# Optimization experiments

Measured on AMD Instinct MI355X. Metric: run time of the kernel, lower is better.

The kernel has to match this reference:

```python
import jax, jax.numpy as jnp
import numpy as np

H, D_IN, D_ATT, D_OUT, S, T = 16, 1024, 64, 64, 2048, 2048


def setup_inputs() -> dict:
    key = jax.random.key(0)
    ks = jax.random.split(key, 12)
    s = lambda fan_in: 1.0 / np.sqrt(fan_in)
    inp = {
        "current_tokens": jax.random.normal(ks[0], (S, D_IN), jnp.float32),
        "context_tokens": jax.random.normal(ks[1], (T, D_IN), jnp.float32),
        # per-head projection weights (stacked over heads)
        "Wq": jax.random.uniform(ks[2], (H, D_IN, D_ATT), jnp.float32, -s(D_IN), s(D_IN)),
        "bq": jax.random.uniform(ks[3], (H, D_ATT), jnp.float32, -s(D_IN), s(D_IN)),
        "Wk": jax.random.uniform(ks[4], (H, D_IN, D_ATT), jnp.float32, -s(D_IN), s(D_IN)),
        "bk": jax.random.uniform(ks[5], (H, D_ATT), jnp.float32, -s(D_IN), s(D_IN)),
        "Wv": jax.random.uniform(ks[6], (H, D_IN, D_OUT), jnp.float32, -s(D_IN), s(D_IN)),
        "bv": jax.random.uniform(ks[7], (H, D_OUT), jnp.float32, -s(D_IN), s(D_IN)),
        # out_proj: Linear(H*D_OUT -> D_OUT)
        "Wo": jax.random.uniform(ks[8], (H * D_OUT, D_OUT), jnp.float32, -s(H * D_OUT), s(H * D_OUT)),
        "bo": jax.random.uniform(ks[9], (D_OUT,), jnp.float32, -s(H * D_OUT), s(H * D_OUT)),
    }
    return inp


def reference(current_tokens, context_tokens, Wq, bq, Wk, bk, Wv, bv, Wo, bo):
    # Batched over heads: q,k: [H,S/T,D_ATT], v: [H,T,D_OUT]
    q = jnp.einsum("si,hid->hsd", current_tokens, Wq) + bq[:, None, :]
    k = jnp.einsum("ti,hid->htd", context_tokens, Wk) + bk[:, None, :]
    v = jnp.einsum("ti,hio->hto", context_tokens, Wv) + bv[:, None, :]
    scores = jnp.einsum("hsd,htd->hst", q, k) / jnp.sqrt(jnp.asarray(D_ATT, q.dtype))
    attn = jax.nn.softmax(scores, axis=-1)          # [H,S,T]
    y = jnp.einsum("hst,hto->hso", attn, v)          # [H,S,D_OUT]
    # torch.cat(ys, dim=0) -> [H*S, D_OUT]; .view(-1, H*D_OUT) -> [S, H*D_OUT]
    # (row-major reshape of head-major stacking, exactly as the torch code does)
    y = y.reshape(-1, D_OUT).reshape(-1, H * D_OUT)
    return y @ Wo + bo                               # [S, D_OUT]
```

## Files before the change

### kernel.cpp

```cpp
#include <hip/hip_runtime.h>

#define DEV static __device__ __forceinline__

typedef unsigned short u16;
typedef unsigned int u32;
typedef float f32x4 __attribute__((ext_vector_type(4)));
typedef __bf16 bf16x8 __attribute__((ext_vector_type(8)));
typedef unsigned short u16x8 __attribute__((ext_vector_type(8)));
typedef unsigned int u32x2 __attribute__((ext_vector_type(2)));
typedef unsigned int u32x4 __attribute__((ext_vector_type(4)));

constexpr int H = 16, DIN = 1024, DH = 64, S = 2048, T = 2048;
constexpr float SM_C = 0.18033688011112042f;

DEV u16 f2bf(float f) { return __builtin_bit_cast(u16, (__bf16)f); }
DEV float bf2f(u16 u) { u32 i = (u32)u << 16; return __builtin_bit_cast(float, i); }
DEV bf16x8 ld_bf8(const u16* p) { return __builtin_bit_cast(bf16x8, *(const u16x8*)p); }
DEV u32 cvtpk(float lo, float hi) {
  u32 r; asm("v_cvt_pk_bf16_f32 %0, %1, %2" : "=v"(r) : "v"(lo), "v"(hi)); return r;
}

#define GLOAD16(gp, lp) __builtin_amdgcn_global_load_lds( \
    (const __attribute__((address_space(1))) void*)(gp),  \
    (__attribute__((address_space(3))) void*)(lp), 16, 0, 0)

__global__ __launch_bounds__(256) void prep_kernel(
    const float* __restrict__ cur, const float* __restrict__ ctx,
    const float* __restrict__ Wq, const float* __restrict__ Wk,
    const float* __restrict__ Wv, const float* __restrict__ Wo,
    u16* __restrict__ cur_bf, u16* __restrict__ ctx_bf,
    u16* __restrict__ WqT, u16* __restrict__ WkvT, u16* __restrict__ WoT) {
  __shared__ alignas(16) float tile[64 * 68];
  int bid = blockIdx.x, tid = threadIdx.x;
  if (bid < 2048) {
    int i = bid * 256 + tid;
    const float* in; u16* out; int j;
    if (i < 262144) { in = cur; out = cur_bf; j = i; }
    else            { in = ctx; out = ctx_bf; j = i - 262144; }
    const float4* p = (const float4*)(in + (size_t)j * 8);
    float4 x = p[0], y = p[1];
    u16x8 o;
    o[0] = f2bf(x.x); o[1] = f2bf(x.y); o[2] = f2bf(x.z); o[3] = f2bf(x.w);
    o[4] = f2bf(y.x); o[5] = f2bf(y.y); o[6] = f2bf(y.z); o[7] = f2bf(y.w);
    *(u16x8*)(out + (size_t)j * 8) = o;
    return;
  }
  int t = bid - 2048, k0 = (t & 15) * 64, y = t >> 4;
  const float* W; u16* Wt; float scale = 1.0f;
  if (y < 16)      { W = Wq + (size_t)y * DIN * DH;        Wt = WqT + (size_t)y * DH * DIN; scale = SM_C; }
  else if (y < 32) { W = Wk + (size_t)(y - 16) * DIN * DH; Wt = WkvT + (size_t)(y - 16) * DH * DIN; }
  else if (y < 48) { W = Wv + (size_t)(y - 32) * DIN * DH; Wt = WkvT + (size_t)(y - 16) * DH * DIN; }
  else             { W = Wo;                               Wt = WoT; }
#pragma unroll
  for (int it = 0; it < 4; ++it) {
    int slot = it * 256 + tid;
    int i = slot >> 4, j4 = (slot & 15) * 4;
    *(float4*)&tile[i * 68 + j4] = *(const float4*)&W[(size_t)(k0 + i) * 64 + j4];
  }
  __syncthreads();
  int n = tid >> 2, kb = (tid & 3) * 16;
  u16x8 o0, o1;
#pragma unroll
  for (int j = 0; j < 8; ++j) o0[j] = f2bf(tile[(kb + j) * 68 + n] * scale);
#pragma unroll
  for (int j = 0; j < 8; ++j) o1[j] = f2bf(tile[(kb + 8 + j) * 68 + n] * scale);
  *(u16x8*)&Wt[(size_t)n * DIN + k0 + kb] = o0;
  *(u16x8*)&Wt[(size_t)n * DIN + k0 + kb + 8] = o1;
}

__global__ __launch_bounds__(256) void gemm_qkv_kernel(
    const u16* __restrict__ Acur, const u16* __restrict__ Actx,
    const u16* __restrict__ WqT, const u16* __restrict__ WkvT,
    const float* __restrict__ bq, const float* __restrict__ bk, const float* __restrict__ bv,
    u16* __restrict__ Qall, u16* __restrict__ Kall, u16* __restrict__ VtAll) {
  __shared__ alignas(16) u16 As[2][128 * 64];
  __shared__ alignas(16) u16 Bs[2][64 * 64];
  int bid = (blockIdx.x & 7) * 96 + (blockIdx.x >> 3);
  const u16 *A, *W; int m0, n0, mode;
  if (bid < 256)      { A = Acur; W = WqT;               m0 = (bid >> 4) * 128;  n0 = (bid & 15) * 64; mode = 0; }
  else if (bid < 512) { int b = bid - 256; A = Actx; W = WkvT;               m0 = (b >> 4) * 128; n0 = (b & 15) * 64; mode = 1; }
  else                { int b = bid - 512; A = Actx; W = WkvT + 1024 * 1024; m0 = (b >> 4) * 128; n0 = (b & 15) * 64; mode = 2; }
  int tid = threadIdx.x, w = tid >> 6, l = tid & 63, g = l >> 4, r = l & 15;
  auto stage = [&](int buf, int kt) {
#pragma unroll
    for (int it = 0; it < 4; ++it) {
      int c = it * 256 + tid, row = c >> 3, q = c & 7;
      GLOAD16(&A[(size_t)(m0 + row) * DIN + kt + ((q ^ (row & 7)) << 3)], &As[buf][c * 8]);
    }
#pragma unroll
    for (int it = 0; it < 2; ++it) {
      int c = it * 256 + tid, row = c >> 3, q = c & 7;
      GLOAD16(&W[(size_t)(n0 + row) * DIN + kt + ((q ^ (row & 7)) << 3)], &Bs[buf][c * 8]);
    }
  };
  stage(0, 0);
  __syncthreads();
  f32x4 acc[2][4] = {};
  for (int t = 0; t < 16; ++t) {
    if (t < 15) stage((t + 1) & 1, (t + 1) * 64);
    int cur = t & 1;
#pragma unroll
    for (int kk = 0; kk < 2; ++kk) {
      int qo = (((kk << 2) | g) ^ (r & 7)) << 3;
      bf16x8 a0 = ld_bf8(&As[cur][(w * 32 + r) * 64 + qo]);
      bf16x8 a1 = ld_bf8(&As[cur][(w * 32 + 16 + r) * 64 + qo]);
      if (mode < 2) {
#pragma unroll
        for (int nf = 0; nf < 4; ++nf) {
          bf16x8 b = ld_bf8(&Bs[cur][(nf * 16 + r) * 64 + qo]);
          acc[0][nf] = __builtin_amdgcn_mfma_f32_16x16x32_bf16(a0, b, acc[0][nf], 0, 0, 0);
          acc[1][nf] = __builtin_amdgcn_mfma_f32_16x16x32_bf16(a1, b, acc[1][nf], 0, 0, 0);
        }
      } else {
#pragma unroll
        for (int nf = 0; nf < 4; ++nf) {
          bf16x8 b = ld_bf8(&Bs[cur][(nf * 16 + r) * 64 + qo]);
          acc[0][nf] = __builtin_amdgcn_mfma_f32_16x16x32_bf16(b, a0, acc[0][nf], 0, 0, 0);
          acc[1][nf] = __builtin_amdgcn_mfma_f32_16x16x32_bf16(b, a1, acc[1][nf], 0, 0, 0);
        }
      }
    }
    __syncthreads();
  }
  if (mode < 2) {
    u16* dst = (mode == 0) ? Qall : Kall;
    const float* bias = (mode == 0) ? bq : bk;
    float bscale = (mode == 0) ? SM_C : 1.0f;
#pragma unroll
    for (int mi = 0; mi < 2; ++mi)
#pragma unroll
      for (int nf = 0; nf < 4; ++nf)
#pragma unroll
        for (int rr = 0; rr < 4; ++rr) {
          int row = m0 + w * 32 + mi * 16 + 4 * g + rr, col = n0 + nf * 16 + r;
          dst[(size_t)row * 1024 + col] = f2bf(acc[mi][nf][rr] + bias[col] * bscale);
        }
  } else {
#pragma unroll
    for (int mi = 0; mi < 2; ++mi)
#pragma unroll
      for (int nf = 0; nf < 4; ++nf)
#pragma unroll
        for (int rr = 0; rr < 4; ++rr) {
          int d = n0 + nf * 16 + 4 * g + rr, tok = m0 + w * 32 + mi * 16 + r;
          VtAll[(size_t)d * 2048 + tok] = f2bf(acc[mi][nf][rr] + bv[d]);
        }
  }
}

__global__ __launch_bounds__(256, 2) void attn_kernel(
    const u16* __restrict__ Qall, const u16* __restrict__ Kall,
    const u16* __restrict__ VtAll, u16* __restrict__ OP, float* __restrict__ LP) {
  int qb = blockIdx.x, h = blockIdx.y, ts = blockIdx.z;
  int tid = threadIdx.x, w = tid >> 6, l = tid & 63, g = l >> 4, r = l & 15;
  __shared__ alignas(16) u16 Ks[2][64 * 64];
  __shared__ alignas(16) u16 Vs[2][64 * 64];
  const int q0 = qb * 256 + w * 64;
  bf16x8 qf[4][2];
#pragma unroll
  for (int sub = 0; sub < 4; ++sub)
#pragma unroll
    for (int kk = 0; kk < 2; ++kk)
      qf[sub][kk] = ld_bf8(&Qall[(size_t)(q0 + sub * 16 + r) * 1024 + h * 64 + kk * 32 + 8 * g]);
  f32x4 o[4][4] = {};
  float lsum[4] = {0.f, 0.f, 0.f, 0.f};
  const int tBeg = ts * 512, tEnd = tBeg + 512;

  auto stage = [&](int buf, int t0) {
#pragma unroll
    for (int it = 0; it < 2; ++it) {
      int c = it * 256 + tid, row = c >> 3, q = c & 7;
      int qs = (q ^ (row & 7)) << 3;
      GLOAD16(&Kall[(size_t)(t0 + row) * 1024 + h * 64 + qs], &Ks[buf][c * 8]);
      GLOAD16(&VtAll[(size_t)(h * 64 + row) * 2048 + t0 + qs], &Vs[buf][c * 8]);
    }
  };
  stage(0, tBeg);
  __syncthreads();
  int cur = 0;
  for (int t0 = tBeg; t0 < tEnd; t0 += 64) {
    if (t0 + 64 < tEnd) stage(cur ^ 1, t0 + 64);
    f32x4 sacc[4][4] = {};
#pragma unroll
    for (int kk = 0; kk < 2; ++kk) {
      int qo = (((kk << 2) | g) ^ (r & 7)) << 3;
#pragma unroll
      for (int nf = 0; nf < 4; ++nf) {
        bf16x8 kf = ld_bf8(&Ks[cur][(nf * 16 + r) * 64 + qo]);
#pragma unroll
        for (int sub = 0; sub < 4; ++sub)
          sacc[sub][nf] = __builtin_amdgcn_mfma_f32_16x16x32_bf16(kf, qf[sub][kk], sacc[sub][nf], 0, 0, 0);
      }
    }
    u32 c[4][4][2];
#pragma unroll
    for (int sub = 0; sub < 4; ++sub)
#pragma unroll
      for (int nf = 0; nf < 4; ++nf) {
        float p0 = __builtin_amdgcn_exp2f(sacc[sub][nf][0]);
        float p1 = __builtin_amdgcn_exp2f(sacc[sub][nf][1]);
        float p2 = __builtin_amdgcn_exp2f(sacc[sub][nf][2]);
        float p3 = __builtin_amdgcn_exp2f(sacc[sub][nf][3]);
        lsum[sub] += (p0 + p1) + (p2 + p3);
        c[sub][nf][0] = cvtpk(p0, p1);
        c[sub][nf][1] = cvtpk(p2, p3);
      }
#pragma unroll
    for (int kk = 0; kk < 2; ++kk) {
      int qo = (((kk << 2) | g) ^ (r & 7)) << 3;
      bf16x8 vf[4];
#pragma unroll
      for (int nf = 0; nf < 4; ++nf) vf[nf] = ld_bf8(&Vs[cur][(nf * 16 + r) * 64 + qo]);
#pragma unroll
      for (int sub = 0; sub < 4; ++sub) {
        u32 dw[4];
#pragma unroll
        for (int s2 = 0; s2 < 2; ++s2) {
          u32x2 t1 = __builtin_amdgcn_permlane32_swap(c[sub][2 * kk][s2], c[sub][2 * kk + 1][s2],
                                                      false, false);
          u32x2 t2 = __builtin_amdgcn_permlane16_swap(t1.x, t1.y, false, false);
          dw[s2] = t2.x; dw[2 + s2] = t2.y;
        }
        bf16x8 pB = __builtin_bit_cast(bf16x8, (u32x4){dw[0], dw[1], dw[2], dw[3]});
#pragma unroll
        for (int nf = 0; nf < 4; ++nf)
          o[sub][nf] = __builtin_amdgcn_mfma_f32_16x16x32_bf16(vf[nf], pB, o[sub][nf], 0, 0, 0);
      }
    }
    __syncthreads();
    cur ^= 1;
  }
#pragma unroll
  for (int sub = 0; sub < 4; ++sub) {
    float ls = lsum[sub];
    ls += __shfl_xor(ls, 16, 64);
    ls += __shfl_xor(ls, 32, 64);
    int s = q0 + sub * 16 + r;
    if (l < 16) LP[(size_t)(ts * 16 + h) * 2048 + s] = ls;
#pragma unroll
    for (int nf = 0; nf < 4; ++nf) {
      uint2 pd;
      pd.x = cvtpk(o[sub][nf][0], o[sub][nf][1]);
      pd.y = cvtpk(o[sub][nf][2], o[sub][nf][3]);
      *(uint2*)&OP[((size_t)(ts * 16 + h) * 2048 + s) * 64 + nf * 16 + 4 * g] = pd;
    }
  }
}

__global__ __launch_bounds__(256) void oproj_part_kernel(const u16* __restrict__ OP,
                                                         const float* __restrict__ LP,
                                                         const u16* __restrict__ WoT,
                                                         float* __restrict__ Part) {
  __shared__ alignas(16) u16 As[128 * 64];
  __shared__ alignas(16) u16 Bs[64 * 64];
  int bx = blockIdx.x, kz = blockIdx.y, kt = kz * 64;
  int tid = threadIdx.x, w = tid >> 6, l = tid & 63, g = l >> 4, r = l & 15;
#pragma unroll
  for (int it = 0; it < 2; ++it) {
    int c = it * 256 + tid, row = c >> 3, q = c & 7;
    GLOAD16(&WoT[(size_t)row * DIN + kt + ((q ^ (row & 7)) << 3)], &Bs[c * 8]);
  }
#pragma unroll
  for (int it = 0; it < 4; ++it) {
    int c = it * 256 + tid, row = c >> 3, q = c & 7, qs = q ^ (row & 7);
    int s = row * 16 + kz;
    float a8[8] = {};
    float lsum = 0.f;
#pragma unroll
    for (int ts = 0; ts < 4; ++ts) {
      u16x8 v = *(const u16x8*)&OP[((size_t)(ts * 16 + bx) * 2048 + s) * 64 + qs * 8];
#pragma unroll
      for (int e = 0; e < 8; ++e) a8[e] += bf2f(v[e]);
      lsum += LP[(size_t)(ts * 16 + bx) * 2048 + s];
    }
    float inv = 1.0f / lsum;
    u16x8 ov;
#pragma unroll
    for (int e = 0; e < 8; ++e) ov[e] = f2bf(a8[e] * inv);
    *(u16x8*)&As[c * 8] = ov;
  }
  __syncthreads();
  f32x4 acc[2][4] = {};
#pragma unroll
  for (int kk = 0; kk < 2; ++kk) {
    int qo = (((kk << 2) | g) ^ (r & 7)) << 3;
    bf16x8 a0 = ld_bf8(&As[(w * 32 + r) * 64 + qo]);
    bf16x8 a1 = ld_bf8(&As[(w * 32 + 16 + r) * 64 + qo]);
#pragma unroll
    for (int nf = 0; nf < 4; ++nf) {
      bf16x8 b = ld_bf8(&Bs[(nf * 16 + r) * 64 + qo]);
      acc[0][nf] = __builtin_amdgcn_mfma_f32_16x16x32_bf16(a0, b, acc[0][nf], 0, 0, 0);
      acc[1][nf] = __builtin_amdgcn_mfma_f32_16x16x32_bf16(a1, b, acc[1][nf], 0, 0, 0);
    }
  }
#pragma unroll
  for (int mi = 0; mi < 2; ++mi)
#pragma unroll
    for (int nf = 0; nf < 4; ++nf)
#pragma unroll
      for (int rr = 0; rr < 4; ++rr)
        Part[((size_t)kz * 2048 + bx * 128 + w * 32 + mi * 16 + 4 * g + rr) * 64 + nf * 16 + r] =
            acc[mi][nf][rr];
}

__global__ __launch_bounds__(256) void oproj_reduce_kernel(const float* __restrict__ Part,
                                                           const float* __restrict__ bo,
                                                           float* __restrict__ out) {
  int i4 = (blockIdx.x * 256 + threadIdx.x) * 4;
  int d = i4 & 63;
  float4 s = {bo[d], bo[d + 1], bo[d + 2], bo[d + 3]};
#pragma unroll
  for (int kz = 0; kz < 16; ++kz) {
    float4 p = *(const float4*)&Part[(size_t)kz * 131072 + i4];
    s.x += p.x; s.y += p.y; s.z += p.z; s.w += p.w;
  }
  *(float4*)&out[i4] = s;
}

extern "C" void kernel_launch(void* const* d_in, const int* in_sizes, int n_in,
                              void* d_out, int out_size, void* d_ws, size_t ws_size,
                              hipStream_t stream) {
  const float* cur = (const float*)d_in[0];
  const float* ctx = (const float*)d_in[1];
  const float* Wq = (const float*)d_in[2];
  const float* bq = (const float*)d_in[3];
  const float* Wk = (const float*)d_in[4];
  const float* bk = (const float*)d_in[5];
  const float* Wv = (const float*)d_in[6];
  const float* bv = (const float*)d_in[7];
  const float* Wo = (const float*)d_in[8];
  const float* bo = (const float*)d_in[9];
  float* out = (float*)d_out;

  char* ws = (char*)d_ws;
  const size_t MB = 1ull << 20;
  u16* cur_bf = (u16*)(ws + 0 * MB);
  u16* ctx_bf = (u16*)(ws + 4 * MB);
  u16* WqT    = (u16*)(ws + 8 * MB);
  u16* WkvT   = (u16*)(ws + 10 * MB);
  u16* WoT    = (u16*)(ws + 14 * MB);
  u16* Qall   = (u16*)(ws + 15 * MB);
  u16* Kall   = (u16*)(ws + 19 * MB);
  u16* VtAll  = (u16*)(ws + 23 * MB);
  u16* OP     = (u16*)(ws + 27 * MB);
  float* LP   = (float*)(ws + 43 * MB);
  float* Part = (float*)(ws + 44 * MB);

  prep_kernel<<<2832, 256, 0, stream>>>(cur, ctx, Wq, Wk, Wv, Wo, cur_bf, ctx_bf,
                                        WqT, WkvT, WoT);
  gemm_qkv_kernel<<<768, 256, 0, stream>>>(cur_bf, ctx_bf, WqT, WkvT, bq, bk, bv,
                                           Qall, Kall, VtAll);
  attn_kernel<<<dim3(8, 16, 4), 256, 0, stream>>>(Qall, Kall, VtAll, OP, LP);
  oproj_part_kernel<<<dim3(16, 16), 256, 0, stream>>>(OP, LP, WoT, Part);
  oproj_reduce_kernel<<<128, 256, 0, stream>>>(Part, bo, out);
}
```

Measured before the change: 67.56 us.

## Load QKV GEMM A operand directly from global into registers, dropping LDS staging

The QKV projection GEMM no longer stages the A tile (activation rows) through shared memory. Each wave loads its own A fragments straight from global memory into registers, double-buffered in registers across k-steps, while B is still staged in LDS. This halves LDS usage and removes the LDS writes and reads for A, which may raise occupancy. In exchange, the per-lane global loads are strided by row rather than coalesced, and more registers are held live.

```diff
diff --git a/kernel.cpp b/kernel.cpp
--- a/kernel.cpp
+++ b/kernel.cpp
@@ -73,7 +73,6 @@
     const u16* __restrict__ WqT, const u16* __restrict__ WkvT,
     const float* __restrict__ bq, const float* __restrict__ bk, const float* __restrict__ bv,
     u16* __restrict__ Qall, u16* __restrict__ Kall, u16* __restrict__ VtAll) {
-  __shared__ alignas(16) u16 As[2][128 * 64];
   __shared__ alignas(16) u16 Bs[2][64 * 64];
   int bid = (blockIdx.x & 7) * 96 + (blockIdx.x >> 3);
   const u16 *A, *W; int m0, n0, mode;
@@ -81,45 +80,53 @@
   else if (bid < 512) { int b = bid - 256; A = Actx; W = WkvT;               m0 = (b >> 4) * 128; n0 = (b & 15) * 64; mode = 1; }
   else                { int b = bid - 512; A = Actx; W = WkvT + 1024 * 1024; m0 = (b >> 4) * 128; n0 = (b & 15) * 64; mode = 2; }
   int tid = threadIdx.x, w = tid >> 6, l = tid & 63, g = l >> 4, r = l & 15;
-  auto stage = [&](int buf, int kt) {
-#pragma unroll
-    for (int it = 0; it < 4; ++it) {
-      int c = it * 256 + tid, row = c >> 3, q = c & 7;
-      GLOAD16(&A[(size_t)(m0 + row) * DIN + kt + ((q ^ (row & 7)) << 3)], &As[buf][c * 8]);
-    }
+  const u16* Abase = A + (size_t)(m0 + w * 32 + r) * DIN + 8 * g;
+  auto stageB = [&](int buf, int kt) {
 #pragma unroll
     for (int it = 0; it < 2; ++it) {
       int c = it * 256 + tid, row = c >> 3, q = c & 7;
       GLOAD16(&W[(size_t)(n0 + row) * DIN + kt + ((q ^ (row & 7)) << 3)], &Bs[buf][c * 8]);
     }
   };
-  stage(0, 0);
-  __syncthreads();
   f32x4 acc[2][4] = {};
-  for (int t = 0; t < 16; ++t) {
-    if (t < 15) stage((t + 1) & 1, (t + 1) * 64);
-    int cur = t & 1;
+  auto loadA = [&](bf16x8 (&a)[2][2], int kt) {
+#pragma unroll
+    for (int mi = 0; mi < 2; ++mi)
+#pragma unroll
+      for (int kk = 0; kk < 2; ++kk)
+        a[mi][kk] = ld_bf8(Abase + (size_t)mi * 16 * DIN + kt + kk * 32);
+  };
+  auto compute = [&](bf16x8 (&a)[2][2], int buf) {
 #pragma unroll
     for (int kk = 0; kk < 2; ++kk) {
       int qo = (((kk << 2) | g) ^ (r & 7)) << 3;
-      bf16x8 a0 = ld_bf8(&As[cur][(w * 32 + r) * 64 + qo]);
-      bf16x8 a1 = ld_bf8(&As[cur][(w * 32 + 16 + r) * 64 + qo]);
-      if (mode < 2) {
-#pragma unroll
-        for (int nf = 0; nf < 4; ++nf) {
-          bf16x8 b = ld_bf8(&Bs[cur][(nf * 16 + r) * 64 + qo]);
-          acc[0][nf] = __builtin_amdgcn_mfma_f32_16x16x32_bf16(a0, b, acc[0][nf], 0, 0, 0);
-          acc[1][nf] = __builtin_amdgcn_mfma_f32_16x16x32_bf16(a1, b, acc[1][nf], 0, 0, 0);
-        }
-      } else {
-#pragma unroll
-        for (int nf = 0; nf < 4; ++nf) {
-          bf16x8 b = ld_bf8(&Bs[cur][(nf * 16 + r) * 64 + qo]);
-          acc[0][nf] = __builtin_amdgcn_mfma_f32_16x16x32_bf16(b, a0, acc[0][nf], 0, 0, 0);
-          acc[1][nf] = __builtin_amdgcn_mfma_f32_16x16x32_bf16(b, a1, acc[1][nf], 0, 0, 0);
+#pragma unroll
+      for (int nf = 0; nf < 4; ++nf) {
+        bf16x8 b = ld_bf8(&Bs[buf][(nf * 16 + r) * 64 + qo]);
+        if (mode < 2) {
+          acc[0][nf] = __builtin_amdgcn_mfma_f32_16x16x32_bf16(a[0][kk], b, acc[0][nf], 0, 0, 0);
+          acc[1][nf] = __builtin_amdgcn_mfma_f32_16x16x32_bf16(a[1][kk], b, acc[1][nf], 0, 0, 0);
+        } else {
+          acc[0][nf] = __builtin_amdgcn_mfma_f32_16x16x32_bf16(b, a[0][kk], acc[0][nf], 0, 0, 0);
+          acc[1][nf] = __builtin_amdgcn_mfma_f32_16x16x32_bf16(b, a[1][kk], acc[1][nf], 0, 0, 0);
         }
       }
     }
+  };
+  bf16x8 aA[2][2], aB[2][2];
+  stageB(0, 0);
+  loadA(aA, 0);
+  __syncthreads();
+  for (int t2 = 0; t2 < 16; t2 += 2) {
+    stageB(1, (t2 + 1) * 64);
+    loadA(aB, (t2 + 1) * 64);
+    compute(aA, 0);
+    __syncthreads();
+    if (t2 + 2 < 16) {
+      stageB(0, (t2 + 2) * 64);
+      loadA(aA, (t2 + 2) * 64);
+    }
+    compute(aB, 1);
     __syncthreads();
   }
   if (mode < 2) {
```

Measured after the change: 78.89 us. 16.8% more time.
